# Performance work log

Hardware: AMD Instinct MI355X
Metric: run time of the kernel (lower is better)

Reference implementation:

```python
import jax, jax.numpy as jnp
import numpy as np

B, L, H = 4, 1024, 8192
NH, HD = 64, 128
PD = HD // 2  # 64, rope-style positional dim
QL = HD * 4 * 3  # 1536, Q latent dim
KVL = HD * 4     # 512, KV latent dim


def setup_inputs() -> dict:
    key = jax.random.key(0)
    ks = jax.random.split(key, 18)
    w = lambda k, i, o: (jax.random.normal(k, (i, o), jnp.float32) * (1.0 / np.sqrt(i))).astype(jnp.float32)
    b = lambda k, o: jnp.zeros((o,), jnp.float32)
    return {
        'x': jax.random.normal(ks[0], (B, L, H), jnp.float32),
        'W_dq': w(ks[1], H, QL),   'b_dq': b(ks[2], QL),
        'W_dkv': w(ks[3], H, KVL), 'b_dkv': b(ks[4], KVL),
        'W_uq': w(ks[5], QL, H),   'b_uq': b(ks[6], H),
        'W_uk': w(ks[7], KVL, H),  'b_uk': b(ks[8], H),
        'W_uv': w(ks[9], KVL, H),  'b_uv': b(ks[10], H),
        'W_pq': w(ks[11], QL, NH * PD), 'b_pq': b(ks[12], NH * PD),
        'W_pk': w(ks[13], H, PD),  'b_pk': b(ks[14], PD),
        'W_o': w(ks[15], H, H),    'b_o': b(ks[16], H),
    }


def reference(x, W_dq, b_dq, W_dkv, b_dkv, W_uq, b_uq, W_uk, b_uk,
              W_uv, b_uv, W_pq, b_pq, W_pk, b_pk, W_o, b_o):
    Bb, Ll, Hh = x.shape
    # low-rank latents
    Q_lat = x @ W_dq + b_dq          # (B, L, 1536)
    KV_lat = x @ W_dkv + b_dkv       # (B, L, 512)
    # up-projections
    Q_c = (Q_lat @ W_uq + b_uq).reshape(Bb, Ll, NH, HD)
    Q_r = (Q_lat @ W_pq + b_pq).reshape(Bb, Ll, NH, PD)
    Q = jnp.concatenate([Q_c, Q_r], axis=-1)            # (B, L, NH, 192)
    K_c = (KV_lat @ W_uk + b_uk).reshape(Bb, Ll, NH, HD)
    K_r = x @ W_pk + b_pk                                # (B, L, 64), shared across heads
    K_r = jnp.broadcast_to(K_r[:, :, None, :], (Bb, Ll, NH, PD))
    K = jnp.concatenate([K_c, K_r], axis=-1)             # (B, L, NH, 192)
    V = (KV_lat @ W_uv + b_uv).reshape(Bb, Ll, NH, HD)   # (B, L, NH, 128)
    # attention with mismatched Q/K (192) vs V (128) head dims; scale by sqrt(128)
    scores = jnp.einsum('bqhd,bkhd->bhqk', Q, K) / np.float32(np.sqrt(HD))
    causal = jnp.tril(jnp.ones((Ll, Ll), bool))
    scores = jnp.where(causal, scores, jnp.float32(-jnp.inf))
    attn = jax.nn.softmax(scores, axis=-1)               # dropout = identity (eval)
    out = jnp.einsum('bhqk,bkhd->bqhd', attn, V).reshape(Bb, Ll, Hh)
    return out @ W_o + b_o
```

## Files before the change

### kernel.cpp

```cpp
#include <hip/hip_runtime.h>
#include <cstdint>

typedef unsigned short u16;
typedef __attribute__((ext_vector_type(8))) short bf16x8;
typedef __attribute__((ext_vector_type(4))) float f32x4;
typedef __attribute__((ext_vector_type(4))) unsigned short u16x4;

__device__ __forceinline__ u16 f2b(float f) {
  union { float f; uint32_t u; } v; v.f = f;
  uint32_t r = v.u + 0x7FFFu + ((v.u >> 16) & 1u);
  return (u16)(r >> 16);
}

__device__ __forceinline__ void gload_lds16(const void* g, void* l) {
  __builtin_amdgcn_global_load_lds((const __attribute__((address_space(1))) void*)g,
                                   (__attribute__((address_space(3))) void*)l, 16, 0, 0);
}

__device__ __forceinline__ void barrier_raw() {
  __builtin_amdgcn_sched_barrier(0);
  asm volatile("" ::: "memory");
  __builtin_amdgcn_s_barrier();
  asm volatile("" ::: "memory");
  __builtin_amdgcn_sched_barrier(0);
}
__device__ __forceinline__ void wait_vm4() {
  asm volatile("s_waitcnt vmcnt(4)" ::: "memory");
  __builtin_amdgcn_sched_barrier(0);
}
__device__ __forceinline__ void wait_lgkm0() {
  asm volatile("s_waitcnt lgkmcnt(0)" ::: "memory");
  __builtin_amdgcn_sched_barrier(0);
}

__global__ __launch_bounds__(256) void cvt_bf16(const float* __restrict__ in,
                                                u16* __restrict__ out, long n) {
  long i = ((long)blockIdx.x * 256 + threadIdx.x) * 4;
  if (i >= n) return;
  f32x4 v = *(const f32x4*)(in + i);
  u16x4 o;
#pragma unroll
  for (int k = 0; k < 4; k++) o[k] = f2b(v[k]);
  *(u16x4*)(out + i) = o;
}

__global__ __launch_bounds__(256) void transpose_cvt(const float* __restrict__ W,
                                                     u16* __restrict__ WT, int K, int N) {
  __shared__ float tile[32][33];
  const int tn0 = blockIdx.x * 32;
  const int tk0 = blockIdx.y * 32;
  const int c = threadIdx.x & 31;
  const int r0 = threadIdx.x >> 5;
#pragma unroll
  for (int rr = 0; rr < 32; rr += 8)
    tile[r0 + rr][c] = W[(long)(tk0 + r0 + rr) * N + tn0 + c];
  __syncthreads();
#pragma unroll
  for (int rr = 0; rr < 32; rr += 8)
    WT[(long)(tn0 + r0 + rr) * K + tk0 + c] = f2b(tile[c][r0 + rr]);
}

__global__ __launch_bounds__(256) void biascat3(const float* __restrict__ a,
                                                const float* __restrict__ b,
                                                const float* __restrict__ c,
                                                float* __restrict__ o) {
  int i = blockIdx.x * 256 + threadIdx.x;
  if (i < 1536) o[i] = a[i];
  else if (i < 2048) o[i] = b[i - 1536];
  else if (i < 2112) o[i] = c[i - 2048];
}
__global__ __launch_bounds__(256) void biascat2(const float* __restrict__ a,
                                                const float* __restrict__ b,
                                                int na, int n, float* __restrict__ o) {
  int i = blockIdx.x * 256 + threadIdx.x;
  if (i >= n) return;
  o[i] = (i < na) ? a[i] : b[i - na];
}

__global__ __launch_bounds__(256) void repl_kr(const u16* __restrict__ Kr,
                                               u16* __restrict__ Kbuf, int stride) {
  long idx = (long)blockIdx.x * 256 + threadIdx.x;
  int d4 = idx & 15;
  long t = idx >> 4;
  int hh = t & 63;
  long tok = t >> 6;
  if (tok >= 4096) return;
  u16x4 v = *(const u16x4*)(Kr + tok * (long)stride + d4 * 4);
  long b = tok >> 10, l = tok & 1023;
  *(u16x4*)(Kbuf + ((b * 64 + hh) * 1024 + l) * 192 + 128 + d4 * 4) = v;
}

template<int MODE>
__global__ __launch_bounds__(512, 2) void gemm256(
    const u16* __restrict__ A, long lda, const u16* __restrict__ BT,
    const float* __restrict__ bias, void* __restrict__ outp, void* __restrict__ outp2,
    int N, int K) {
  __shared__ u16 sA[2][2][8192];
  __shared__ u16 sB[2][2][8192];
  const int tid = threadIdx.x;
  const int lane = tid & 63;
  const int w = tid >> 6;
  const int wr = w >> 2, wc = w & 3;
  const int hi = lane >> 4, lo = lane & 15;

  const int Nt = gridDim.x, Mt = gridDim.y;
  const int bid = blockIdx.y * Nt + blockIdx.x;
  const int xcd = bid & 7;
  const int idx = bid >> 3;
  int mt, nt;
  if ((Nt & 1) == 0) {
    const int Rm = Mt >> 2, Rn = Nt >> 1;
    const int xr = xcd & 3, xcn = xcd >> 2;
    const int Wb = Rn < 8 ? Rn : 8;
    const int cb = idx / (Rm * Wb);
    const int rem = idx - cb * (Rm * Wb);
    mt = xr * Rm + (rem % Rm);
    nt = xcn * Rn + cb * Wb + rem / Rm;
  } else {
    const int Rm = Mt >> 3;
    const int Wb = Nt < 8 ? Nt : 8;
    const int cb = idx / (Rm * Wb);
    const int rem = idx - cb * (Rm * Wb);
    mt = xcd * Rm + (rem % Rm);
    nt = cb * Wb + rem / Rm;
  }
  const long m0 = (long)mt * 256;
  const long n0 = (long)nt * 256;

  const int nkt = K >> 6;

  const int srow = tid >> 2;
  const int scol = ((tid & 3) ^ ((tid >> 3) & 3)) * 8;
  const long arow0 = m0 + srow, arow1 = arow0 + 128;
  long brow0 = n0 + srow, brow1 = brow0 + 128;
  if (brow0 > N - 1) brow0 = N - 1;
  if (brow1 > N - 1) brow1 = N - 1;
  const u16* aS0 = A + arow0 * lda + scol;
  const u16* aS1 = A + arow1 * lda + scol;
  const u16* bS0 = BT + brow0 * (long)K + scol;
  const u16* bS1 = BT + brow1 * (long)K + scol;

  const int aRd = (wr * 128 + lo) * 32 + (hi ^ ((lo >> 1) & 3)) * 8;
  const int bRd = (wc * 64 + lo) * 32 + (hi ^ ((lo >> 1) & 3)) * 8;

  f32x4 acc[8][4] = {};

#define STAGE(s0, s1, koff, dst) do { \
    gload_lds16((s0) + (koff), (dst) + tid * 8); \
    gload_lds16((s1) + (koff), (dst) + 4096 + tid * 8); \
  } while (0)
#define LDA_F(bufr, kh, m) (*(const bf16x8*)(&sA[bufr][kh][aRd + (m) * 512]))
#define LDB_F(bufr, kh, n) (*(const bf16x8*)(&sB[bufr][kh][bRd + (n) * 512]))
#define MFMA_GRP(mi, av) \
    acc[mi][0] = __builtin_amdgcn_mfma_f32_16x16x32_bf16(av, b0, acc[mi][0], 0, 0, 0); \
    acc[mi][1] = __builtin_amdgcn_mfma_f32_16x16x32_bf16(av, b1, acc[mi][1], 0, 0, 0); \
    acc[mi][2] = __builtin_amdgcn_mfma_f32_16x16x32_bf16(av, b2, acc[mi][2], 0, 0, 0); \
    acc[mi][3] = __builtin_amdgcn_mfma_f32_16x16x32_bf16(av, b3, acc[mi][3], 0, 0, 0);

  STAGE(aS0, aS1, 0, &sA[0][0][0]);
  STAGE(bS0, bS1, 0, &sB[0][0][0]);
  STAGE(aS0, aS1, 32, &sA[0][1][0]);
  STAGE(bS0, bS1, 32, &sB[0][1][0]);
  wait_vm4();
  barrier_raw();

  for (int t = 0; t < nkt; ++t) {
    const int cur = t & 1, nxt = cur ^ 1;
    const int t1c = (t + 1 < nkt) ? t + 1 : nkt - 1;
    const long o1 = (long)t1c * 64;
    bf16x8 b0, b1, b2, b3, a0, a1, a2, a3, a4, a5, a6, a7;
    b0 = LDB_F(cur, 0, 0); b1 = LDB_F(cur, 0, 1); b2 = LDB_F(cur, 0, 2); b3 = LDB_F(cur, 0, 3);
    a0 = LDA_F(cur, 0, 0); a1 = LDA_F(cur, 0, 1); a2 = LDA_F(cur, 0, 2); a3 = LDA_F(cur, 0, 3);
    STAGE(aS0, aS1, o1, &sA[nxt][0][0]);
    barrier_raw();
    wait_lgkm0();
    __builtin_amdgcn_s_setprio(1);
    MFMA_GRP(0, a0) MFMA_GRP(1, a1) MFMA_GRP(2, a2) MFMA_GRP(3, a3)
    __builtin_amdgcn_s_setprio(0);
    barrier_raw();
    a4 = LDA_F(cur, 0, 4); a5 = LDA_F(cur, 0, 5); a6 = LDA_F(cur, 0, 6); a7 = LDA_F(cur, 0, 7);
    STAGE(bS0, bS1, o1, &sB[nxt][0][0]);
    wait_vm4();
    barrier_raw();
    wait_lgkm0();
    __builtin_amdgcn_s_setprio(1);
    MFMA_GRP(4, a4) MFMA_GRP(5, a5) MFMA_GRP(6, a6) MFMA_GRP(7, a7)
    __builtin_amdgcn_s_setprio(0);
    barrier_raw();
    b0 = LDB_F(cur, 1, 0); b1 = LDB_F(cur, 1, 1); b2 = LDB_F(cur, 1, 2); b3 = LDB_F(cur, 1, 3);
    a0 = LDA_F(cur, 1, 0); a1 = LDA_F(cur, 1, 1); a2 = LDA_F(cur, 1, 2); a3 = LDA_F(cur, 1, 3);
    STAGE(aS0, aS1, o1 + 32, &sA[nxt][1][0]);
    barrier_raw();
    wait_lgkm0();
    __builtin_amdgcn_s_setprio(1);
    MFMA_GRP(0, a0) MFMA_GRP(1, a1) MFMA_GRP(2, a2) MFMA_GRP(3, a3)
    __builtin_amdgcn_s_setprio(0);
    barrier_raw();
    a4 = LDA_F(cur, 1, 4); a5 = LDA_F(cur, 1, 5); a6 = LDA_F(cur, 1, 6); a7 = LDA_F(cur, 1, 7);
    STAGE(bS0, bS1, o1 + 32, &sB[nxt][1][0]);
    wait_vm4();
    barrier_raw();
    wait_lgkm0();
    __builtin_amdgcn_s_setprio(1);
    MFMA_GRP(4, a4) MFMA_GRP(5, a5) MFMA_GRP(6, a6) MFMA_GRP(7, a7)
    __builtin_amdgcn_s_setprio(0);
    barrier_raw();
  }
  asm volatile("s_waitcnt vmcnt(0)" ::: "memory");

#undef STAGE
#undef LDA_F
#undef LDB_F
#undef MFMA_GRP

#pragma unroll
  for (int m = 0; m < 8; m++) {
#pragma unroll
    for (int n = 0; n < 4; n++) {
      const long mb = m0 + wr * 128 + m * 16 + hi * 4;
      const long nn = n0 + wc * 64 + n * 16 + lo;
      if (nn >= N) continue;
      const float bv = bias[nn];
      if (MODE == 0) {
#pragma unroll
        for (int r = 0; r < 4; r++)
          ((u16*)outp)[(mb + r) * (long)N + nn] = f2b(acc[m][n][r] + bv);
      } else if (MODE == 3) {
#pragma unroll
        for (int r = 0; r < 4; r++)
          ((float*)outp)[(mb + r) * (long)N + nn] = acc[m][n][r] + bv;
      } else if (MODE == 4) {
        if (nn < 8192) {
          const long h = nn >> 7, d = nn & 127;
#pragma unroll
          for (int r = 0; r < 4; r++) {
            const long mm = mb + r;
            const long bq = mm >> 10, l = mm & 1023;
            ((u16*)outp)[((bq * 64 + h) * 1024 + l) * 192 + d] = f2b(acc[m][n][r] + bv);
          }
        } else {
          const long q = nn - 8192;
          const long h = q >> 6, d = q & 63;
#pragma unroll
          for (int r = 0; r < 4; r++) {
            const long mm = mb + r;
            const long bq = mm >> 10, l = mm & 1023;
            ((u16*)outp)[((bq * 64 + h) * 1024 + l) * 192 + 128 + d] = f2b(acc[m][n][r] + bv);
          }
        }
      } else {
        if (nn < 8192) {
          const long h = nn >> 7, d = nn & 127;
#pragma unroll
          for (int r = 0; r < 4; r++) {
            const long mm = mb + r;
            const long bq = mm >> 10, l = mm & 1023;
            ((u16*)outp)[((bq * 64 + h) * 1024 + l) * 192 + d] = f2b(acc[m][n][r] + bv);
          }
        } else {
          const long v = nn - 8192;
          const long h = v >> 7, d = v & 127;
          u16x4 pk;
#pragma unroll
          for (int r = 0; r < 4; r++) pk[r] = f2b(acc[m][n][r] + bv);
          const long bq = mb >> 10, l = mb & 1023;
          *(u16x4*)((u16*)outp2 + ((bq * 64 + h) * 128 + d) * 1024 + l) = pk;
        }
      }
    }
  }
}

__global__ __launch_bounds__(512, 2) void attn256(const u16* __restrict__ Qb,
                                                  const u16* __restrict__ Kb,
                                                  const u16* __restrict__ Vt,
                                                  u16* __restrict__ O) {
  __shared__ u16 sK[2][12288];
  __shared__ u16 sV[2][8192];
  __shared__ u16 P[8][32][72];
  const int bh = blockIdx.x;
  const int qtb = 3 - blockIdx.y;
  const int b = bh >> 6, h = bh & 63;
  const int tid = threadIdx.x, w = tid >> 6, lane = tid & 63;
  const int hi = lane >> 4, lo = lane & 15, lo7 = lane & 7;
  const int q0w = qtb * 256 + w * 32;
  const u16* Qh = Qb + (size_t)bh * 1024 * 192;
  const u16* Kh = Kb + (size_t)bh * 1024 * 192;
  const u16* Vh = Vt + (size_t)bh * 128 * 1024;
  const float scale = 0.08838834764831845f;
  const float NEGINF = -3.0e38f;

  int kOff0, kOff1, kOff2, vOff0, vOff1;
  {
    int g0 = tid, g1 = tid + 512, g2 = tid + 1024;
    int r0 = g0 / 24, r1 = g1 / 24, r2 = g2 / 24;
    kOff0 = r0 * 192 + ((g0 - r0 * 24) ^ (r0 & 7)) * 8;
    kOff1 = r1 * 192 + ((g1 - r1 * 24) ^ (r1 & 7)) * 8;
    kOff2 = r2 * 192 + ((g2 - r2 * 24) ^ (r2 & 7)) * 8;
    int s0 = tid, s1 = tid + 512;
    vOff0 = (s0 >> 3) * 1024 + ((s0 & 7) ^ ((s0 >> 3) & 7)) * 8;
    vOff1 = (s1 >> 3) * 1024 + ((s1 & 7) ^ ((s1 >> 3) & 7)) * 8;
  }
#define STAGE_KV(tt, bb) do { \
    const u16* kb_ = Kh + (size_t)(tt) * (64 * 192); \
    const u16* vb_ = Vh + (size_t)(tt) * 64; \
    gload_lds16(kb_ + kOff0, &sK[bb][0] + tid * 8); \
    gload_lds16(kb_ + kOff1, &sK[bb][4096] + tid * 8); \
    gload_lds16(kb_ + kOff2, &sK[bb][8192] + tid * 8); \
    gload_lds16(vb_ + vOff0, &sV[bb][0] + tid * 8); \
    gload_lds16(vb_ + vOff1, &sV[bb][4096] + tid * 8); \
  } while (0)

  bf16x8 qf[2][6];
#pragma unroll
  for (int qi = 0; qi < 2; qi++) {
    const u16* qp = Qh + (size_t)(q0w + qi * 16 + lo) * 192 + hi * 8;
#pragma unroll
    for (int f = 0; f < 6; f++) qf[qi][f] = *(const bf16x8*)(qp + f * 32);
  }

  f32x4 oacc[2][8] = {};
  float m_run[2][4], l_run[2][4];
#pragma unroll
  for (int qi = 0; qi < 2; qi++)
#pragma unroll
    for (int r = 0; r < 4; r++) { m_run[qi][r] = NEGINF; l_run[qi][r] = 0.f; }

  const int nkt = (qtb + 1) * 4;
  STAGE_KV(0, 0);
  __syncthreads();

  for (int t = 0; t < nkt; t++) {
    const int cur = t & 1;
    const int tn = (t + 1 < nkt) ? t + 1 : nkt - 1;
    STAGE_KV(tn, cur ^ 1);
    const int k0 = t * 64;
    if (k0 < q0w + 32) {
      f32x4 s[2][4] = {};
      __builtin_amdgcn_s_setprio(1);
#pragma unroll
      for (int j = 0; j < 4; j++) {
#pragma unroll
        for (int f = 0; f < 6; f++) {
          bf16x8 kf = *(const bf16x8*)(&sK[cur][((j * 16 + lo) * 24 + ((f * 4 + hi) ^ lo7)) * 8]);
          s[0][j] = __builtin_amdgcn_mfma_f32_16x16x32_bf16(qf[0][f], kf, s[0][j], 0, 0, 0);
          s[1][j] = __builtin_amdgcn_mfma_f32_16x16x32_bf16(qf[1][f], kf, s[1][j], 0, 0, 0);
        }
      }
      __builtin_amdgcn_s_setprio(0);
      const bool diag = (k0 + 63 > q0w);
#pragma unroll
      for (int qi = 0; qi < 2; qi++) {
#pragma unroll
        for (int r = 0; r < 4; r++) {
          const int q = q0w + qi * 16 + hi * 4 + r;
          float sv[4];
          float mx = NEGINF;
#pragma unroll
          for (int j = 0; j < 4; j++) {
            float v = s[qi][j][r] * scale;
            if (diag && (k0 + j * 16 + lo > q)) v = NEGINF;
            sv[j] = v;
            mx = fmaxf(mx, v);
          }
#pragma unroll
          for (int o = 1; o < 16; o <<= 1) mx = fmaxf(mx, __shfl_xor(mx, o, 64));
          const float mnew = fmaxf(m_run[qi][r], mx);
          float sum = 0.f;
#pragma unroll
          for (int j = 0; j < 4; j++) {
            float pv = __expf(sv[j] - mnew);
            sum += pv;
            P[w][qi * 16 + hi * 4 + r][j * 16 + lo] = f2b(pv);
          }
#pragma unroll
          for (int o = 1; o < 16; o <<= 1) sum += __shfl_xor(sum, o, 64);
          const float alpha = __expf(m_run[qi][r] - mnew);
          l_run[qi][r] = l_run[qi][r] * alpha + sum;
          m_run[qi][r] = mnew;
#pragma unroll
          for (int j = 0; j < 8; j++) oacc[qi][j][r] *= alpha;
        }
      }
      __builtin_amdgcn_s_setprio(1);
#pragma unroll
      for (int kk = 0; kk < 2; kk++) {
        bf16x8 pf0 = *(const bf16x8*)(&P[w][lo][kk * 32 + hi * 8]);
        bf16x8 pf1 = *(const bf16x8*)(&P[w][16 + lo][kk * 32 + hi * 8]);
#pragma unroll
        for (int j = 0; j < 8; j++) {
          bf16x8 vf = *(const bf16x8*)(&sV[cur][((j * 16 + lo) * 8 + ((kk * 4 + hi) ^ lo7)) * 8]);
          oacc[0][j] = __builtin_amdgcn_mfma_f32_16x16x32_bf16(pf0, vf, oacc[0][j], 0, 0, 0);
          oacc[1][j] = __builtin_amdgcn_mfma_f32_16x16x32_bf16(pf1, vf, oacc[1][j], 0, 0, 0);
        }
      }
      __builtin_amdgcn_s_setprio(0);
    }
    __syncthreads();
  }
#undef STAGE_KV

#pragma unroll
  for (int qi = 0; qi < 2; qi++) {
#pragma unroll
    for (int r = 0; r < 4; r++) {
      const float inv = 1.f / l_run[qi][r];
      const int q = q0w + qi * 16 + hi * 4 + r;
      u16* op = O + ((size_t)(b * 1024 + q) * 64 + h) * 128;
#pragma unroll
      for (int j = 0; j < 8; j++)
        op[j * 16 + lo] = f2b(oacc[qi][j][r] * inv);
    }
  }
}

extern "C" void kernel_launch(void* const* d_in, const int* in_sizes, int n_in,
                              void* d_out, int out_size, void* d_ws, size_t ws_size,
                              hipStream_t stream) {
  const float* x     = (const float*)d_in[0];
  const float* W_dq  = (const float*)d_in[1];
  const float* b_dq  = (const float*)d_in[2];
  const float* W_dkv = (const float*)d_in[3];
  const float* b_dkv = (const float*)d_in[4];
  const float* W_uq  = (const float*)d_in[5];
  const float* b_uq  = (const float*)d_in[6];
  const float* W_uk  = (const float*)d_in[7];
  const float* b_uk  = (const float*)d_in[8];
  const float* W_uv  = (const float*)d_in[9];
  const float* b_uv  = (const float*)d_in[10];
  const float* W_pq  = (const float*)d_in[11];
  const float* b_pq  = (const float*)d_in[12];
  const float* W_pk  = (const float*)d_in[13];
  const float* b_pk  = (const float*)d_in[14];
  const float* W_o   = (const float*)d_in[15];
  const float* b_o   = (const float*)d_in[16];

  char* ws = (char*)d_ws;
  size_t off = 0;
  auto alloc = [&](size_t bytes) {
    char* p = ws + off;
    off += (bytes + 255) & ~(size_t)255;
    return p;
  };
  u16* xbf   = (u16*)alloc(33554432ULL * 2);
  u16* WT    = (u16*)alloc(67108864ULL * 2);
  u16* lat   = (u16*)alloc(4096ULL * 2112 * 2);
  float* bct = (float*)alloc(2112ULL * 4);
  float* bq  = (float*)alloc(12288ULL * 4);
  float* bkv = (float*)alloc(16384ULL * 4);
  u16* Qbuf  = (u16*)alloc(100663296ULL);
  u16* Kbuf  = (u16*)alloc(100663296ULL);
  u16* Vt    = (u16*)alloc(67108864ULL);
  u16* Obuf  = xbf;
  if (off > ws_size) return;

  dim3 blk(256), blk5(512);
  cvt_bf16<<<dim3(32768), blk, 0, stream>>>(x, xbf, 33554432L);
  transpose_cvt<<<dim3(48, 256), blk, 0, stream>>>(W_dq, WT, 8192, 1536);
  transpose_cvt<<<dim3(16, 256), blk, 0, stream>>>(W_dkv, WT + 1536L * 8192, 8192, 512);
  transpose_cvt<<<dim3(2, 256), blk, 0, stream>>>(W_pk, WT + 2048L * 8192, 8192, 64);
  biascat3<<<dim3(9), blk, 0, stream>>>(b_dq, b_dkv, b_pk, bct);
  gemm256<0><<<dim3(9, 16), blk5, 0, stream>>>(xbf, 8192, WT, bct, lat, nullptr, 2112, 8192);
  repl_kr<<<dim3(16384), blk, 0, stream>>>(lat + 2048, Kbuf, 2112);
  transpose_cvt<<<dim3(256, 48), blk, 0, stream>>>(W_uq, WT, 1536, 8192);
  transpose_cvt<<<dim3(128, 48), blk, 0, stream>>>(W_pq, WT + 8192L * 1536, 1536, 4096);
  biascat2<<<dim3(48), blk, 0, stream>>>(b_uq, b_pq, 8192, 12288, bq);
  gemm256<4><<<dim3(48, 16), blk5, 0, stream>>>(lat, 2112, WT, bq, Qbuf, nullptr, 12288, 1536);
  transpose_cvt<<<dim3(256, 16), blk, 0, stream>>>(W_uk, WT, 512, 8192);
  transpose_cvt<<<dim3(256, 16), blk, 0, stream>>>(W_uv, WT + 8192L * 512, 512, 8192);
  biascat2<<<dim3(64), blk, 0, stream>>>(b_uk, b_uv, 8192, 16384, bkv);
  gemm256<5><<<dim3(64, 16), blk5, 0, stream>>>(lat + 1536, 2112, WT, bkv, Kbuf, Vt, 16384, 512);
  attn256<<<dim3(256, 4), blk5, 0, stream>>>(Qbuf, Kbuf, Vt, Obuf);
  transpose_cvt<<<dim3(256, 256), blk, 0, stream>>>(W_o, WT, 8192, 8192);
  gemm256<3><<<dim3(32, 16), blk5, 0, stream>>>(Obuf, 8192, WT, b_o, d_out, nullptr, 8192, 8192);
}
```

Baseline: 1.524 ms.

## Restructure GEMM main loop into quadrant MFMA schedule with deeper prefetch

Reorganizes the gemm256 inner loop so each phase computes a 4x2 quadrant of accumulators across both k-halves, reusing A and B fragments from registers, and issues global-to-LDS loads two k-tiles ahead instead of one. It also adds an explicit ldb parameter for the B operand stride, which all call sites set to K. The goal is to cut LDS reads per MFMA and overlap global loads with compute better. In exchange it raises register pressure and makes the buffer reuse timing more delicate, since the next tile's first half is written into the current buffer.

```diff
diff --git a/kernel.cpp b/kernel.cpp
--- a/kernel.cpp
+++ b/kernel.cpp
@@ -92,7 +92,7 @@
 
 template<int MODE>
 __global__ __launch_bounds__(512, 2) void gemm256(
-    const u16* __restrict__ A, long lda, const u16* __restrict__ BT,
+    const u16* __restrict__ A, long lda, const u16* __restrict__ BT, long ldb,
     const float* __restrict__ bias, void* __restrict__ outp, void* __restrict__ outp2,
     int N, int K) {
   __shared__ u16 sA[2][2][8192];
@@ -137,8 +137,8 @@
   if (brow1 > N - 1) brow1 = N - 1;
   const u16* aS0 = A + arow0 * lda + scol;
   const u16* aS1 = A + arow1 * lda + scol;
-  const u16* bS0 = BT + brow0 * (long)K + scol;
-  const u16* bS1 = BT + brow1 * (long)K + scol;
+  const u16* bS0 = BT + brow0 * ldb + scol;
+  const u16* bS1 = BT + brow1 * ldb + scol;
 
   const int aRd = (wr * 128 + lo) * 32 + (hi ^ ((lo >> 1) & 3)) * 8;
   const int bRd = (wc * 64 + lo) * 32 + (hi ^ ((lo >> 1) & 3)) * 8;
@@ -149,69 +149,81 @@
     gload_lds16((s0) + (koff), (dst) + tid * 8); \
     gload_lds16((s1) + (koff), (dst) + 4096 + tid * 8); \
   } while (0)
-#define LDA_F(bufr, kh, m) (*(const bf16x8*)(&sA[bufr][kh][aRd + (m) * 512]))
-#define LDB_F(bufr, kh, n) (*(const bf16x8*)(&sB[bufr][kh][bRd + (n) * 512]))
-#define MFMA_GRP(mi, av) \
-    acc[mi][0] = __builtin_amdgcn_mfma_f32_16x16x32_bf16(av, b0, acc[mi][0], 0, 0, 0); \
-    acc[mi][1] = __builtin_amdgcn_mfma_f32_16x16x32_bf16(av, b1, acc[mi][1], 0, 0, 0); \
-    acc[mi][2] = __builtin_amdgcn_mfma_f32_16x16x32_bf16(av, b2, acc[mi][2], 0, 0, 0); \
-    acc[mi][3] = __builtin_amdgcn_mfma_f32_16x16x32_bf16(av, b3, acc[mi][3], 0, 0, 0);
+#define LD_A(kst, m) (*(const bf16x8*)(&sA[cur][kst][aRd + (m) * 512]))
+#define LD_B(kst, n) (*(const bf16x8*)(&sB[cur][kst][bRd + (n) * 512]))
+#define MF(d, av, bv) d = __builtin_amdgcn_mfma_f32_16x16x32_bf16(av, bv, d, 0, 0, 0)
+#define QUAD(R0, C0, B00, B01, B10, B11) \
+    MF(acc[R0+0][C0+0], a00, B00); MF(acc[R0+0][C0+0], a01, B01); \
+    MF(acc[R0+0][C0+1], a00, B10); MF(acc[R0+0][C0+1], a01, B11); \
+    MF(acc[R0+1][C0+0], a10, B00); MF(acc[R0+1][C0+0], a11, B01); \
+    MF(acc[R0+1][C0+1], a10, B10); MF(acc[R0+1][C0+1], a11, B11); \
+    MF(acc[R0+2][C0+0], a20, B00); MF(acc[R0+2][C0+0], a21, B01); \
+    MF(acc[R0+2][C0+1], a20, B10); MF(acc[R0+2][C0+1], a21, B11); \
+    MF(acc[R0+3][C0+0], a30, B00); MF(acc[R0+3][C0+0], a31, B01); \
+    MF(acc[R0+3][C0+1], a30, B10); MF(acc[R0+3][C0+1], a31, B11);
 
   STAGE(aS0, aS1, 0, &sA[0][0][0]);
   STAGE(bS0, bS1, 0, &sB[0][0][0]);
   STAGE(aS0, aS1, 32, &sA[0][1][0]);
   STAGE(bS0, bS1, 32, &sB[0][1][0]);
+  {
+    const long t1o = (nkt > 1) ? 64 : 0;
+    STAGE(bS0, bS1, t1o, &sB[1][0][0]);
+    STAGE(aS0, aS1, t1o, &sA[1][0][0]);
+  }
   wait_vm4();
   barrier_raw();
 
   for (int t = 0; t < nkt; ++t) {
     const int cur = t & 1, nxt = cur ^ 1;
     const int t1c = (t + 1 < nkt) ? t + 1 : nkt - 1;
+    const int t2c = (t + 2 < nkt) ? t + 2 : nkt - 1;
     const long o1 = (long)t1c * 64;
-    bf16x8 b0, b1, b2, b3, a0, a1, a2, a3, a4, a5, a6, a7;
-    b0 = LDB_F(cur, 0, 0); b1 = LDB_F(cur, 0, 1); b2 = LDB_F(cur, 0, 2); b3 = LDB_F(cur, 0, 3);
-    a0 = LDA_F(cur, 0, 0); a1 = LDA_F(cur, 0, 1); a2 = LDA_F(cur, 0, 2); a3 = LDA_F(cur, 0, 3);
-    STAGE(aS0, aS1, o1, &sA[nxt][0][0]);
+    const long o2 = (long)t2c * 64;
+    bf16x8 a00, a01, a10, a11, a20, a21, a30, a31;
+    bf16x8 b000, b001, b010, b011;
+    bf16x8 b100, b101, b110, b111;
+    a00 = LD_A(0, 0); a01 = LD_A(1, 0); a10 = LD_A(0, 1); a11 = LD_A(1, 1);
+    a20 = LD_A(0, 2); a21 = LD_A(1, 2); a30 = LD_A(0, 3); a31 = LD_A(1, 3);
+    b000 = LD_B(0, 0); b001 = LD_B(1, 0); b010 = LD_B(0, 1); b011 = LD_B(1, 1);
+    STAGE(aS0, aS1, o1 + 32, &sA[nxt][1][0]);
     barrier_raw();
     wait_lgkm0();
     __builtin_amdgcn_s_setprio(1);
-    MFMA_GRP(0, a0) MFMA_GRP(1, a1) MFMA_GRP(2, a2) MFMA_GRP(3, a3)
+    QUAD(0, 0, b000, b001, b010, b011)
     __builtin_amdgcn_s_setprio(0);
     barrier_raw();
-    a4 = LDA_F(cur, 0, 4); a5 = LDA_F(cur, 0, 5); a6 = LDA_F(cur, 0, 6); a7 = LDA_F(cur, 0, 7);
-    STAGE(bS0, bS1, o1, &sB[nxt][0][0]);
-    wait_vm4();
+    b100 = LD_B(0, 2); b101 = LD_B(1, 2); b110 = LD_B(0, 3); b111 = LD_B(1, 3);
+    STAGE(bS0, bS1, o1 + 32, &sB[nxt][1][0]);
     barrier_raw();
     wait_lgkm0();
     __builtin_amdgcn_s_setprio(1);
-    MFMA_GRP(4, a4) MFMA_GRP(5, a5) MFMA_GRP(6, a6) MFMA_GRP(7, a7)
+    QUAD(0, 2, b100, b101, b110, b111)
     __builtin_amdgcn_s_setprio(0);
     barrier_raw();
-    b0 = LDB_F(cur, 1, 0); b1 = LDB_F(cur, 1, 1); b2 = LDB_F(cur, 1, 2); b3 = LDB_F(cur, 1, 3);
-    a0 = LDA_F(cur, 1, 0); a1 = LDA_F(cur, 1, 1); a2 = LDA_F(cur, 1, 2); a3 = LDA_F(cur, 1, 3);
-    STAGE(aS0, aS1, o1 + 32, &sA[nxt][1][0]);
+    a00 = LD_A(0, 4); a01 = LD_A(1, 4); a10 = LD_A(0, 5); a11 = LD_A(1, 5);
+    a20 = LD_A(0, 6); a21 = LD_A(1, 6); a30 = LD_A(0, 7); a31 = LD_A(1, 7);
+    STAGE(bS0, bS1, o2, &sB[cur][0][0]);
     barrier_raw();
     wait_lgkm0();
     __builtin_amdgcn_s_setprio(1);
-    MFMA_GRP(0, a0) MFMA_GRP(1, a1) MFMA_GRP(2, a2) MFMA_GRP(3, a3)
+    QUAD(4, 2, b100, b101, b110, b111)
     __builtin_amdgcn_s_setprio(0);
     barrier_raw();
-    a4 = LDA_F(cur, 1, 4); a5 = LDA_F(cur, 1, 5); a6 = LDA_F(cur, 1, 6); a7 = LDA_F(cur, 1, 7);
-    STAGE(bS0, bS1, o1 + 32, &sB[nxt][1][0]);
+    STAGE(aS0, aS1, o2, &sA[cur][0][0]);
+    __builtin_amdgcn_s_setprio(1);
+    QUAD(4, 0, b000, b001, b010, b011)
+    __builtin_amdgcn_s_setprio(0);
     wait_vm4();
     barrier_raw();
-    wait_lgkm0();
-    __builtin_amdgcn_s_setprio(1);
-    MFMA_GRP(4, a4) MFMA_GRP(5, a5) MFMA_GRP(6, a6) MFMA_GRP(7, a7)
-    __builtin_amdgcn_s_setprio(0);
-    barrier_raw();
   }
   asm volatile("s_waitcnt vmcnt(0)" ::: "memory");
 
 #undef STAGE
-#undef LDA_F
-#undef LDB_F
-#undef MFMA_GRP
+#undef LD_A
+#undef LD_B
+#undef MF
+#undef QUAD
 
 #pragma unroll
   for (int m = 0; m < 8; m++) {
@@ -460,17 +472,17 @@
   transpose_cvt<<<dim3(16, 256), blk, 0, stream>>>(W_dkv, WT + 1536L * 8192, 8192, 512);
   transpose_cvt<<<dim3(2, 256), blk, 0, stream>>>(W_pk, WT + 2048L * 8192, 8192, 64);
   biascat3<<<dim3(9), blk, 0, stream>>>(b_dq, b_dkv, b_pk, bct);
-  gemm256<0><<<dim3(9, 16), blk5, 0, stream>>>(xbf, 8192, WT, bct, lat, nullptr, 2112, 8192);
+  gemm256<0><<<dim3(9, 16), blk5, 0, stream>>>(xbf, 8192, WT, 8192, bct, lat, nullptr, 2112, 8192);
   repl_kr<<<dim3(16384), blk, 0, stream>>>(lat + 2048, Kbuf, 2112);
   transpose_cvt<<<dim3(256, 48), blk, 0, stream>>>(W_uq, WT, 1536, 8192);
   transpose_cvt<<<dim3(128, 48), blk, 0, stream>>>(W_pq, WT + 8192L * 1536, 1536, 4096);
   biascat2<<<dim3(48), blk, 0, stream>>>(b_uq, b_pq, 8192, 12288, bq);
-  gemm256<4><<<dim3(48, 16), blk5, 0, stream>>>(lat, 2112, WT, bq, Qbuf, nullptr, 12288, 1536);
+  gemm256<4><<<dim3(48, 16), blk5, 0, stream>>>(lat, 2112, WT, 1536, bq, Qbuf, nullptr, 12288, 1536);
   transpose_cvt<<<dim3(256, 16), blk, 0, stream>>>(W_uk, WT, 512, 8192);
   transpose_cvt<<<dim3(256, 16), blk, 0, stream>>>(W_uv, WT + 8192L * 512, 512, 8192);
   biascat2<<<dim3(64), blk, 0, stream>>>(b_uk, b_uv, 8192, 16384, bkv);
-  gemm256<5><<<dim3(64, 16), blk5, 0, stream>>>(lat + 1536, 2112, WT, bkv, Kbuf, Vt, 16384, 512);
+  gemm256<5><<<dim3(64, 16), blk5, 0, stream>>>(lat + 1536, 2112, WT, 512, bkv, Kbuf, Vt, 16384, 512);
   attn256<<<dim3(256, 4), blk5, 0, stream>>>(Qbuf, Kbuf, Vt, Obuf);
   transpose_cvt<<<dim3(256, 256), blk, 0, stream>>>(W_o, WT, 8192, 8192);
-  gemm256<3><<<dim3(32, 16), blk5, 0, stream>>>(Obuf, 8192, WT, b_o, d_out, nullptr, 8192, 8192);
-}
+  gemm256<3><<<dim3(32, 16), blk5, 0, stream>>>(Obuf, 8192, WT, 8192, b_o, d_out, nullptr, 8192, 8192);
+}
```

New measurement: 1.593 ms. 1.05x slower.
